# Kernel tuning notes

Hardware: AMD Instinct MI355X
Metric: run time of the kernel (lower is better)

## Reference

```python
import jax, jax.numpy as jnp
import numpy as np

NUM_AGENTS = 16


def setup_inputs() -> dict:
    key = jax.random.key(0)
    ks = jax.random.split(key, 9)
    B, N, C = 64, 1024, 512
    w_scale = 1.0 / np.sqrt(C)  # keep pre-softmax logits in a sane range
    return {
        "x": jax.random.normal(ks[0], (B, N, C), dtype=jnp.float32),
        "Wq": jax.random.normal(ks[1], (C, C), dtype=jnp.float32) * w_scale,
        "bq": jax.random.normal(ks[2], (C,), dtype=jnp.float32) * 0.02,
        "Wk": jax.random.normal(ks[3], (C, C), dtype=jnp.float32) * w_scale,
        "bk": jax.random.normal(ks[4], (C,), dtype=jnp.float32) * 0.02,
        "Wv": jax.random.normal(ks[5], (C, C), dtype=jnp.float32) * w_scale,
        "bv": jax.random.normal(ks[6], (C,), dtype=jnp.float32) * 0.02,
        "Wo": jax.random.normal(ks[7], (C, C), dtype=jnp.float32) * w_scale,
        "bo": jax.random.normal(ks[8], (C,), dtype=jnp.float32) * 0.02,
    }


def reference(x, Wq, bq, Wk, bk, Wv, bv, Wo, bo):
    B, N, C = x.shape
    M = NUM_AGENTS
    scale = C ** (-0.5)
    # torch nn.Linear: y = x @ W.T + b
    Q = jnp.einsum('bnc,dc->bnd', x, Wq) + bq  # [B,N,C]
    K = jnp.einsum('bnc,dc->bnd', x, Wk) + bk
    V = jnp.einsum('bnc,dc->bnd', x, Wv) + bv
    # adaptive_avg_pool1d over token dim; N % M == 0 -> mean over groups of N//M
    A = Q.reshape(B, M, N // M, C).mean(axis=2)  # [B,M,C]
    # stage 1: softmax(Q A^T)
    agent_tokens = jax.nn.softmax(jnp.einsum('bnc,bmc->bnm', Q, A) * scale, axis=-1)  # [B,N,M]
    # stage 2: softmax(A K^T) V
    agent_features = jax.nn.softmax(jnp.einsum('bmc,bnc->bmn', A, K) * scale, axis=-1)  # [B,M,N]
    agent_features = jnp.einsum('bmn,bnc->bmc', agent_features, V)  # [B,M,C]
    # combine
    agent_attn = jnp.einsum('bnm,bmc->bnc', agent_tokens, agent_features)  # [B,N,C]
    return jnp.einsum('bnc,dc->bnd', agent_attn, Wo) + bo
```

## Files before the change

### kernel.cpp

```cpp
#include <hip/hip_runtime.h>

#define BB 64
#define NN 1024
#define CC 512
#define MM 16
#define SCALE 0.04419417382415922f

__device__ __forceinline__ float dot4(float4 a, float4 b) {
  return a.x*b.x + a.y*b.y + a.z*b.z + a.w*b.w;
}

__global__ __launch_bounds__(128) void k_pool3(const float* __restrict__ x,
                                               float* __restrict__ P) {
  __shared__ float4 tmp[64];
  int bm = blockIdx.x, ch = blockIdx.y, t = threadIdx.x;
  int col = t & 63, p = t >> 6;
  const float4* base = (const float4*)(x + (size_t)bm*64*CC) + ch*64;
  float4 a = {0.f,0.f,0.f,0.f};
  #pragma unroll 8
  for (int i = 0; i < 32; ++i) {
    float4 v = base[(size_t)(p*32 + i)*128 + col];
    a.x += v.x; a.y += v.y; a.z += v.z; a.w += v.w;
  }
  if (p == 1) tmp[col] = a;
  __syncthreads();
  if (p == 0) {
    float4 o = tmp[col];
    const float inv = 1.0f/64.0f;
    float4 r = {(a.x+o.x)*inv, (a.y+o.y)*inv, (a.z+o.z)*inv, (a.w+o.w)*inv};
    ((float4*)P)[(size_t)bm*128 + ch*64 + col] = r;
  }
}

__global__ __launch_bounds__(256) void k_gemm_nt4(const float* __restrict__ In,
    const float* __restrict__ W, const float* __restrict__ bias,
    float* __restrict__ Out) {
  __shared__ float Is[64*36];
  __shared__ float Ws[64*36];
  int t = threadIdx.x;
  int dblk = blockIdx.x, rblk = blockIdx.y, kz = blockIdx.z;
  int td = t & 15, tr = t >> 4;
  float acc[4][4];
  #pragma unroll
  for (int i = 0; i < 4; ++i)
    #pragma unroll
    for (int j = 0; j < 4; ++j) acc[i][j] = 0.f;
  const float4* In4 = (const float4*)In;
  const float4* W4  = (const float4*)W;
  for (int chk = 0; chk < 4; ++chk) {
    int kc = kz*32 + chk*8;
    __syncthreads();
    #pragma unroll
    for (int p = 0; p < 2; ++p) {
      int i = p*256 + t;
      int r = i >> 3, cc = i & 7;
      float4 v = In4[(size_t)(rblk*64 + r)*128 + kc + cc];
      *(float4*)&Is[r*36 + cc*4] = v;
      float4 w = W4[(size_t)(dblk*64 + r)*128 + kc + cc];
      *(float4*)&Ws[r*36 + cc*4] = w;
    }
    __syncthreads();
    #pragma unroll
    for (int cc = 0; cc < 8; ++cc) {
      float4 a0 = *(float4*)&Is[(tr*4+0)*36 + cc*4];
      float4 a1 = *(float4*)&Is[(tr*4+1)*36 + cc*4];
      float4 a2 = *(float4*)&Is[(tr*4+2)*36 + cc*4];
      float4 a3 = *(float4*)&Is[(tr*4+3)*36 + cc*4];
      float4 w0 = *(float4*)&Ws[(td*4+0)*36 + cc*4];
      float4 w1 = *(float4*)&Ws[(td*4+1)*36 + cc*4];
      float4 w2 = *(float4*)&Ws[(td*4+2)*36 + cc*4];
      float4 w3 = *(float4*)&Ws[(td*4+3)*36 + cc*4];
      acc[0][0] += dot4(a0,w0); acc[0][1] += dot4(a0,w1);
      acc[0][2] += dot4(a0,w2); acc[0][3] += dot4(a0,w3);
      acc[1][0] += dot4(a1,w0); acc[1][1] += dot4(a1,w1);
      acc[1][2] += dot4(a1,w2); acc[1][3] += dot4(a1,w3);
      acc[2][0] += dot4(a2,w0); acc[2][1] += dot4(a2,w1);
      acc[2][2] += dot4(a2,w2); acc[2][3] += dot4(a2,w3);
      acc[3][0] += dot4(a3,w0); acc[3][1] += dot4(a3,w1);
      acc[3][2] += dot4(a3,w2); acc[3][3] += dot4(a3,w3);
    }
  }
  int r0 = rblk*64 + tr*4, d0 = dblk*64 + td*4;
  if (kz == 0) {
    #pragma unroll
    for (int j = 0; j < 4; ++j) {
      float bj = bias[d0+j];
      #pragma unroll
      for (int i = 0; i < 4; ++i) acc[i][j] += bj;
    }
  }
  #pragma unroll
  for (int i = 0; i < 4; ++i)
    #pragma unroll
    for (int j = 0; j < 4; ++j)
      atomicAdd(&Out[(size_t)(r0+i)*CC + d0 + j], acc[i][j]);
}

__global__ void k_abqk(const float* __restrict__ A, const float* __restrict__ bq,
                       const float* __restrict__ bk, float* __restrict__ abq,
                       float* __restrict__ abk) {
  int bm = blockIdx.x, t = threadIdx.x;
  float sq = 0.f, sk = 0.f;
  for (int d = t; d < CC; d += 64) {
    float a = A[(size_t)bm*CC + d];
    sq += a*bq[d]; sk += a*bk[d];
  }
  #pragma unroll
  for (int off = 32; off >= 1; off >>= 1) {
    sq += __shfl_xor(sq, off);
    sk += __shfl_xor(sk, off);
  }
  if (t == 0) { abq[bm] = sq; abk[bm] = sk; }
}

__global__ __launch_bounds__(256) void k_gemm_nn3(const float* __restrict__ A,
    const float* __restrict__ Wq, const float* __restrict__ Wk,
    float* __restrict__ Aq, float* __restrict__ Ak) {
  __shared__ float As[4*512];
  int t = threadIdx.x;
  int rblk = blockIdx.y, cblk = blockIdx.x;
  const float4* A4 = (const float4*)A;
  float4* As4 = (float4*)As;
  #pragma unroll
  for (int k = 0; k < 2; ++k) {
    int i = k*256 + t;
    As4[i] = A4[(size_t)(rblk*4 + (i>>7))*128 + (i&127)];
  }
  __syncthreads();
  int c4 = cblk*64 + (t & 63);
  int rr = t >> 6;
  const float* Ar = &As[rr*512];
  const float4* Wq4 = (const float4*)Wq;
  const float4* Wk4 = (const float4*)Wk;
  float4 accq = {0.f,0.f,0.f,0.f}, acck = {0.f,0.f,0.f,0.f};
  #pragma unroll 8
  for (int d = 0; d < 512; ++d) {
    float a = Ar[d];
    float4 wq = Wq4[(size_t)d*128 + c4];
    float4 wk = Wk4[(size_t)d*128 + c4];
    accq.x += a*wq.x; accq.y += a*wq.y; accq.z += a*wq.z; accq.w += a*wq.w;
    acck.x += a*wk.x; acck.y += a*wk.y; acck.z += a*wk.z; acck.w += a*wk.w;
  }
  int row = rblk*4 + rr;
  ((float4*)Aq)[(size_t)row*128 + c4] = accq;
  ((float4*)Ak)[(size_t)row*128 + c4] = acck;
}

__global__ __launch_bounds__(256) void k_mega(const float* __restrict__ x,
    const float* __restrict__ Aq, const float* __restrict__ Ak,
    const float* __restrict__ abq, const float* __restrict__ abk,
    float* __restrict__ PT, float* __restrict__ dpart,
    float* __restrict__ Spart) {
  __shared__ float Es[64*16];
  __shared__ float ds2[128];
  int ns = blockIdx.x, b = blockIdx.y, t = threadIdx.x;
  int n0 = ns*64;
  int ci = t & 15, tw = t >> 4;
  const float4* Aq4 = (const float4*)(Aq + (size_t)b*MM*CC);
  const float4* Ak4 = (const float4*)(Ak + (size_t)b*MM*CC);
  for (int pass = 0; pass < 4; ++pass) {
    int tok = pass*16 + tw;
    int n = n0 + tok;
    const float4* xr = (const float4*)(x + ((size_t)b*NN + n)*CC);
    float aq[MM], ak[MM];
    #pragma unroll
    for (int m = 0; m < MM; ++m) { aq[m] = 0.f; ak[m] = 0.f; }
    #pragma unroll 4
    for (int k = 0; k < 8; ++k) {
      float4 xv = xr[k*16 + ci];
      #pragma unroll
      for (int m = 0; m < MM; ++m) {
        aq[m] += dot4(xv, Aq4[m*128 + k*16 + ci]);
        ak[m] += dot4(xv, Ak4[m*128 + k*16 + ci]);
      }
    }
    #pragma unroll
    for (int off = 1; off < 16; off <<= 1) {
      #pragma unroll
      for (int m = 0; m < MM; ++m) {
        aq[m] += __shfl_xor(aq[m], off);
        ak[m] += __shfl_xor(ak[m], off);
      }
    }
    if (ci == 0) {
      float mx = -1e30f;
      #pragma unroll
      for (int m = 0; m < MM; ++m) {
        aq[m] = SCALE*(aq[m] + abq[b*MM + m]);
        mx = fmaxf(mx, aq[m]);
      }
      float s = 0.f;
      #pragma unroll
      for (int m = 0; m < MM; ++m) { aq[m] = expf(aq[m]-mx); s += aq[m]; }
      float inv = 1.0f/s;
      float4* PT4 = (float4*)(PT + ((size_t)b*NN + n)*MM);
      #pragma unroll
      for (int j = 0; j < 4; ++j) {
        float4 v = {aq[j*4+0]*inv, aq[j*4+1]*inv, aq[j*4+2]*inv, aq[j*4+3]*inv};
        PT4[j] = v;
      }
      float e[MM];
      #pragma unroll
      for (int m = 0; m < MM; ++m)
        e[m] = expf(SCALE*(ak[m] + abk[b*MM + m]));
      float4* er = (float4*)&Es[tok*MM];
      #pragma unroll
      for (int j = 0; j < 4; ++j) {
        float4 v = {e[j*4+0], e[j*4+1], e[j*4+2], e[j*4+3]};
        er[j] = v;
      }
    }
  }
  __syncthreads();
  if (t < 128) {
    int m = t >> 3, j = t & 7;
    float p = 0.f;
    #pragma unroll
    for (int i = 0; i < 8; ++i) p += Es[(j*8 + i)*MM + m];
    ds2[m*8 + j] = p;
  }
  __syncthreads();
  if (t < MM) {
    float d = 0.f;
    #pragma unroll
    for (int j = 0; j < 8; ++j) d += ds2[t*8 + j];
    dpart[(size_t)ns*NN + b*MM + t] = d;
  }
  int c2 = t;
  float2 acc[MM];
  #pragma unroll
  for (int m = 0; m < MM; ++m) acc[m] = make_float2(0.f, 0.f);
  const float2* xb = (const float2*)(x + ((size_t)b*NN + n0)*CC);
  #pragma unroll 4
  for (int nl = 0; nl < 64; ++nl) {
    float2 xv = xb[(size_t)nl*256 + c2];
    #pragma unroll
    for (int m = 0; m < MM; ++m) {
      float e = Es[nl*MM + m];
      acc[m].x += e*xv.x; acc[m].y += e*xv.y;
    }
  }
  float2* Sp2 = (float2*)Spart;
  #pragma unroll
  for (int m = 0; m < MM; ++m)
    Sp2[(((size_t)ns*BB + b)*MM + m)*256 + c2] = acc[m];
}

__global__ void k_sreduce3(const float* __restrict__ Spart,
                           const float* __restrict__ dpart,
                           float* __restrict__ S) {
  int idx = blockIdx.x*256 + threadIdx.x;
  int row = idx >> 7;
  const float4* Sp4 = (const float4*)Spart;
  float4 a = {0.f,0.f,0.f,0.f};
  #pragma unroll
  for (int ns = 0; ns < 16; ++ns) {
    float4 v = Sp4[((size_t)ns*NN + row)*128 + (idx & 127)];
    a.x += v.x; a.y += v.y; a.z += v.z; a.w += v.w;
  }
  float d = 0.f;
  #pragma unroll
  for (int ns = 0; ns < 16; ++ns) d += dpart[(size_t)ns*NN + row];
  float inv = 1.0f/d;
  float4 r = {a.x*inv, a.y*inv, a.z*inv, a.w*inv};
  ((float4*)S)[idx] = r;
}

__global__ __launch_bounds__(256) void k_final5(const float* __restrict__ PT,
                                                const float* __restrict__ G,
                                                float* __restrict__ out) {
  __shared__ float ps[32*MM];
  int nc = blockIdx.x, b = blockIdx.y, t = threadIdx.x;
  int col = t & 127, h = t >> 7;
  int n0 = nc*32;
  if (t < 128)
    ((float4*)ps)[t] = ((const float4*)(PT + ((size_t)b*NN + n0)*MM))[t];
  float4 g[MM];
  const float4* G4 = (const float4*)(G + (size_t)b*MM*CC);
  #pragma unroll
  for (int m = 0; m < MM; ++m) g[m] = G4[m*128 + col];
  __syncthreads();
  float4* out4 = (float4*)(out + ((size_t)b*NN + n0 + h*16)*CC);
  for (int i = 0; i < 16; ++i) {
    float4 o = {0.f,0.f,0.f,0.f};
    #pragma unroll
    for (int m = 0; m < MM; ++m) {
      float p = ps[(h*16 + i)*MM + m];
      o.x += p*g[m].x; o.y += p*g[m].y; o.z += p*g[m].z; o.w += p*g[m].w;
    }
    out4[(size_t)i*128 + col] = o;
  }
}

extern "C" void kernel_launch(void* const* d_in, const int* in_sizes, int n_in,
                              void* d_out, int out_size, void* d_ws, size_t ws_size,
                              hipStream_t stream) {
  (void)in_sizes; (void)n_in; (void)out_size; (void)ws_size;
  const float* x  = (const float*)d_in[0];
  const float* Wq = (const float*)d_in[1];
  const float* bq = (const float*)d_in[2];
  const float* Wk = (const float*)d_in[3];
  const float* bk = (const float*)d_in[4];
  const float* Wv = (const float*)d_in[5];
  const float* bv = (const float*)d_in[6];
  const float* Wo = (const float*)d_in[7];
  const float* bo = (const float*)d_in[8];
  float* out = (float*)d_out;

  float* ws  = (float*)d_ws;
  float* P     = ws;
  float* A     = P  + 1024*512;
  float* Aq    = A  + 1024*512;
  float* Ak    = Aq + 1024*512;
  float* abq   = Ak + 1024*512;
  float* abk   = abq + 1024;
  float* PT    = abk + 1024;
  float* dpart = PT + 1024*1024;
  float* S     = dpart + 16*1024;
  float* AF    = S  + 1024*512;
  float* G     = AF + 1024*512;
  float* Spart = G  + 1024*512;

  hipMemsetAsync(A,  0, (size_t)1024*512*sizeof(float), stream);
  hipMemsetAsync(AF, 0, (size_t)1024*512*sizeof(float), stream);
  hipMemsetAsync(G,  0, (size_t)1024*512*sizeof(float), stream);

  k_pool3<<<dim3(1024,2), 128, 0, stream>>>(x, P);
  k_gemm_nt4<<<dim3(8,16,4), 256, 0, stream>>>(P, Wq, bq, A);
  k_abqk<<<1024, 64, 0, stream>>>(A, bq, bk, abq, abk);
  k_gemm_nn3<<<dim3(2,256), 256, 0, stream>>>(A, Wq, Wk, Aq, Ak);
  k_mega<<<dim3(16,64), 256, 0, stream>>>(x, Aq, Ak, abq, abk, PT, dpart, Spart);
  k_sreduce3<<<512, 256, 0, stream>>>(Spart, dpart, S);
  k_gemm_nt4<<<dim3(8,16,4), 256, 0, stream>>>(S, Wv, bv, AF);
  k_gemm_nt4<<<dim3(8,16,4), 256, 0, stream>>>(AF, Wo, bo, G);
  k_final5<<<dim3(32,64), 256, 0, stream>>>(PT, G, out);
}
```

Measured before the change: 741.9 us.

## Fuse bias-dot kernel into GEMM, widen mega kernel to 512 threads, merge memsets

Removes the separate k_abqk launch by computing A·bq and A·bk inside k_gemm_nn3 from the shared-memory tile. k_mega now runs 512 threads per block. Each half of the block accumulates a separate 32-token slice of the E·x reduction, which doubles the number of Spart partials that k_sreduce3 must sum. The PT softmax output is staged through padded shared memory so it can be written with coalesced float4 stores. The workspace is reordered so the three zeroing memsets become one. The cost is more partial-sum traffic and higher register pressure from launch_bounds(512,8).

```diff
diff --git a/kernel.cpp b/kernel.cpp
--- a/kernel.cpp
+++ b/kernel.cpp
@@ -96,26 +96,11 @@
       atomicAdd(&Out[(size_t)(r0+i)*CC + d0 + j], acc[i][j]);
 }
 
-__global__ void k_abqk(const float* __restrict__ A, const float* __restrict__ bq,
-                       const float* __restrict__ bk, float* __restrict__ abq,
-                       float* __restrict__ abk) {
-  int bm = blockIdx.x, t = threadIdx.x;
-  float sq = 0.f, sk = 0.f;
-  for (int d = t; d < CC; d += 64) {
-    float a = A[(size_t)bm*CC + d];
-    sq += a*bq[d]; sk += a*bk[d];
-  }
-  #pragma unroll
-  for (int off = 32; off >= 1; off >>= 1) {
-    sq += __shfl_xor(sq, off);
-    sk += __shfl_xor(sk, off);
-  }
-  if (t == 0) { abq[bm] = sq; abk[bm] = sk; }
-}
-
 __global__ __launch_bounds__(256) void k_gemm_nn3(const float* __restrict__ A,
     const float* __restrict__ Wq, const float* __restrict__ Wk,
-    float* __restrict__ Aq, float* __restrict__ Ak) {
+    const float* __restrict__ bq, const float* __restrict__ bk,
+    float* __restrict__ Aq, float* __restrict__ Ak,
+    float* __restrict__ abq, float* __restrict__ abk) {
   __shared__ float As[4*512];
   int t = threadIdx.x;
   int rblk = blockIdx.y, cblk = blockIdx.x;
@@ -127,6 +112,22 @@
     As4[i] = A4[(size_t)(rblk*4 + (i>>7))*128 + (i&127)];
   }
   __syncthreads();
+  if (cblk == 0 && t < 64) {
+    int row = t >> 4, seg = t & 15;
+    float sq = 0.f, sk = 0.f;
+    #pragma unroll 8
+    for (int i = 0; i < 32; ++i) {
+      float a = As[row*512 + seg*32 + i];
+      sq += a*bq[seg*32 + i];
+      sk += a*bk[seg*32 + i];
+    }
+    #pragma unroll
+    for (int off = 1; off < 16; off <<= 1) {
+      sq += __shfl_xor(sq, off);
+      sk += __shfl_xor(sk, off);
+    }
+    if (seg == 0) { abq[rblk*4 + row] = sq; abk[rblk*4 + row] = sk; }
+  }
   int c4 = cblk*64 + (t & 63);
   int rr = t >> 6;
   const float* Ar = &As[rr*512];
@@ -146,20 +147,21 @@
   ((float4*)Ak)[(size_t)row*128 + c4] = acck;
 }
 
-__global__ __launch_bounds__(256) void k_mega(const float* __restrict__ x,
+__global__ __launch_bounds__(512, 8) void k_mega(const float* __restrict__ x,
     const float* __restrict__ Aq, const float* __restrict__ Ak,
     const float* __restrict__ abq, const float* __restrict__ abk,
     float* __restrict__ PT, float* __restrict__ dpart,
     float* __restrict__ Spart) {
-  __shared__ float Es[64*16];
+  __shared__ float Es[64*20];
+  __shared__ float Ps[64*20];
   __shared__ float ds2[128];
   int ns = blockIdx.x, b = blockIdx.y, t = threadIdx.x;
   int n0 = ns*64;
   int ci = t & 15, tw = t >> 4;
   const float4* Aq4 = (const float4*)(Aq + (size_t)b*MM*CC);
   const float4* Ak4 = (const float4*)(Ak + (size_t)b*MM*CC);
-  for (int pass = 0; pass < 4; ++pass) {
-    int tok = pass*16 + tw;
+  for (int pass = 0; pass < 2; ++pass) {
+    int tok = pass*32 + tw;
     int n = n0 + tok;
     const float4* xr = (const float4*)(x + ((size_t)b*NN + n)*CC);
     float aq[MM], ak[MM];
@@ -193,30 +195,25 @@
       #pragma unroll
       for (int m = 0; m < MM; ++m) { aq[m] = expf(aq[m]-mx); s += aq[m]; }
       float inv = 1.0f/s;
-      float4* PT4 = (float4*)(PT + ((size_t)b*NN + n)*MM);
-      #pragma unroll
-      for (int j = 0; j < 4; ++j) {
-        float4 v = {aq[j*4+0]*inv, aq[j*4+1]*inv, aq[j*4+2]*inv, aq[j*4+3]*inv};
-        PT4[j] = v;
-      }
-      float e[MM];
+      #pragma unroll
+      for (int m = 0; m < MM; ++m) Ps[tok*20 + m] = aq[m]*inv;
       #pragma unroll
       for (int m = 0; m < MM; ++m)
-        e[m] = expf(SCALE*(ak[m] + abk[b*MM + m]));
-      float4* er = (float4*)&Es[tok*MM];
-      #pragma unroll
-      for (int j = 0; j < 4; ++j) {
-        float4 v = {e[j*4+0], e[j*4+1], e[j*4+2], e[j*4+3]};
-        er[j] = v;
-      }
-    }
-  }
-  __syncthreads();
+        Es[tok*20 + m] = expf(SCALE*(ak[m] + abk[b*MM + m]));
+    }
+  }
+  __syncthreads();
+  if (t < 256) {
+    int tok = t >> 2, q = t & 3;
+    float4 v = {Ps[tok*20 + q*4+0], Ps[tok*20 + q*4+1],
+                Ps[tok*20 + q*4+2], Ps[tok*20 + q*4+3]};
+    ((float4*)PT)[((size_t)b*NN + n0 + tok)*4 + q] = v;
+  }
   if (t < 128) {
     int m = t >> 3, j = t & 7;
     float p = 0.f;
     #pragma unroll
-    for (int i = 0; i < 8; ++i) p += Es[(j*8 + i)*MM + m];
+    for (int i = 0; i < 8; ++i) p += Es[(j*8 + i)*20 + m];
     ds2[m*8 + j] = p;
   }
   __syncthreads();
@@ -226,24 +223,41 @@
     for (int j = 0; j < 8; ++j) d += ds2[t*8 + j];
     dpart[(size_t)ns*NN + b*MM + t] = d;
   }
-  int c2 = t;
+  int c2 = t & 255, h = t >> 8;
   float2 acc[MM];
   #pragma unroll
   for (int m = 0; m < MM; ++m) acc[m] = make_float2(0.f, 0.f);
-  const float2* xb = (const float2*)(x + ((size_t)b*NN + n0)*CC);
-  #pragma unroll 4
-  for (int nl = 0; nl < 64; ++nl) {
+  const float2* xb = (const float2*)(x + ((size_t)b*NN + n0 + h*32)*CC);
+  #pragma unroll 2
+  for (int nl = 0; nl < 32; ++nl) {
     float2 xv = xb[(size_t)nl*256 + c2];
-    #pragma unroll
-    for (int m = 0; m < MM; ++m) {
-      float e = Es[nl*MM + m];
-      acc[m].x += e*xv.x; acc[m].y += e*xv.y;
-    }
+    const float* er = &Es[(h*32 + nl)*20];
+    float4 e0 = *(const float4*)&er[0];
+    float4 e1 = *(const float4*)&er[4];
+    float4 e2 = *(const float4*)&er[8];
+    float4 e3 = *(const float4*)&er[12];
+    acc[0].x += e0.x*xv.x; acc[0].y += e0.x*xv.y;
+    acc[1].x += e0.y*xv.x; acc[1].y += e0.y*xv.y;
+    acc[2].x += e0.z*xv.x; acc[2].y += e0.z*xv.y;
+    acc[3].x += e0.w*xv.x; acc[3].y += e0.w*xv.y;
+    acc[4].x += e1.x*xv.x; acc[4].y += e1.x*xv.y;
+    acc[5].x += e1.y*xv.x; acc[5].y += e1.y*xv.y;
+    acc[6].x += e1.z*xv.x; acc[6].y += e1.z*xv.y;
+    acc[7].x += e1.w*xv.x; acc[7].y += e1.w*xv.y;
+    acc[8].x += e2.x*xv.x; acc[8].y += e2.x*xv.y;
+    acc[9].x += e2.y*xv.x; acc[9].y += e2.y*xv.y;
+    acc[10].x += e2.z*xv.x; acc[10].y += e2.z*xv.y;
+    acc[11].x += e2.w*xv.x; acc[11].y += e2.w*xv.y;
+    acc[12].x += e3.x*xv.x; acc[12].y += e3.x*xv.y;
+    acc[13].x += e3.y*xv.x; acc[13].y += e3.y*xv.y;
+    acc[14].x += e3.z*xv.x; acc[14].y += e3.z*xv.y;
+    acc[15].x += e3.w*xv.x; acc[15].y += e3.w*xv.y;
   }
   float2* Sp2 = (float2*)Spart;
+  int ns2 = ns*2 + h;
   #pragma unroll
   for (int m = 0; m < MM; ++m)
-    Sp2[(((size_t)ns*BB + b)*MM + m)*256 + c2] = acc[m];
+    Sp2[(((size_t)ns2*BB + b)*MM + m)*256 + c2] = acc[m];
 }
 
 __global__ void k_sreduce3(const float* __restrict__ Spart,
@@ -254,8 +268,8 @@
   const float4* Sp4 = (const float4*)Spart;
   float4 a = {0.f,0.f,0.f,0.f};
   #pragma unroll
-  for (int ns = 0; ns < 16; ++ns) {
-    float4 v = Sp4[((size_t)ns*NN + row)*128 + (idx & 127)];
+  for (int ns2 = 0; ns2 < 32; ++ns2) {
+    float4 v = Sp4[((size_t)ns2*NN + row)*128 + (idx & 127)];
     a.x += v.x; a.y += v.y; a.z += v.z; a.w += v.w;
   }
   float d = 0.f;
@@ -310,26 +324,22 @@
   float* ws  = (float*)d_ws;
   float* P     = ws;
   float* A     = P  + 1024*512;
-  float* Aq    = A  + 1024*512;
+  float* AF    = A  + 1024*512;
+  float* G     = AF + 1024*512;
+  float* Aq    = G  + 1024*512;
   float* Ak    = Aq + 1024*512;
   float* abq   = Ak + 1024*512;
   float* abk   = abq + 1024;
   float* PT    = abk + 1024;
   float* dpart = PT + 1024*1024;
   float* S     = dpart + 16*1024;
-  float* AF    = S  + 1024*512;
-  float* G     = AF + 1024*512;
-  float* Spart = G  + 1024*512;
-
-  hipMemsetAsync(A,  0, (size_t)1024*512*sizeof(float), stream);
-  hipMemsetAsync(AF, 0, (size_t)1024*512*sizeof(float), stream);
-  hipMemsetAsync(G,  0, (size_t)1024*512*sizeof(float), stream);
-
+  float* Spart = S + 1024*512;
+
+  hipMemsetAsync(A, 0, (size_t)3*1024*512*sizeof(float), stream);
   k_pool3<<<dim3(1024,2), 128, 0, stream>>>(x, P);
   k_gemm_nt4<<<dim3(8,16,4), 256, 0, stream>>>(P, Wq, bq, A);
-  k_abqk<<<1024, 64, 0, stream>>>(A, bq, bk, abq, abk);
-  k_gemm_nn3<<<dim3(2,256), 256, 0, stream>>>(A, Wq, Wk, Aq, Ak);
-  k_mega<<<dim3(16,64), 256, 0, stream>>>(x, Aq, Ak, abq, abk, PT, dpart, Spart);
+  k_gemm_nn3<<<dim3(2,256), 256, 0, stream>>>(A, Wq, Wk, bq, bk, Aq, Ak, abq, abk);
+  k_mega<<<dim3(16,64), 512, 0, stream>>>(x, Aq, Ak, abq, abk, PT, dpart, Spart);
   k_sreduce3<<<512, 256, 0, stream>>>(Spart, dpart, S);
   k_gemm_nt4<<<dim3(8,16,4), 256, 0, stream>>>(S, Wv, bv, AF);
   k_gemm_nt4<<<dim3(8,16,4), 256, 0, stream>>>(AF, Wo, bo, G);
```

New measurement: 639.9 us. -13.7%, faster.
